# Kernel tuning notes

Measured on AMD Instinct MI355X. Metric: run time of the kernel, lower is better.

Reference implementation:

```python
import jax, jax.numpy as jnp
import numpy as np

NQ = 7
DIM = 2 ** NQ  # 128
N_LAYERS = 3

# Pauli-Z sign tables over the 128 basis states (wire 0 = most significant bit)
_bits = ((np.arange(DIM)[None, :] >> (NQ - 1 - np.arange(NQ)[:, None])) & 1)
_SZ = (1.0 - 2.0 * _bits).astype(np.float32)            # [7, 128]
_SZZ = (_SZ * np.roll(_SZ, -1, axis=0)).astype(np.float32)  # [7, 128], Z_i Z_{(i+1)%7}


def _cnot_perm(c, t):
    # CNOT is a basis-state permutation: flip target bit where control bit = 1
    k = np.arange(DIM)
    return k ^ (((k >> (NQ - 1 - c)) & 1) << (NQ - 1 - t))


def _apply_ry(state, theta, q):
    # state: [B, 128] complex64; theta: [B] or scalar (real)
    B = state.shape[0]
    s = state.reshape(B, 2 ** q, 2, 2 ** (NQ - 1 - q))
    c = jnp.reshape(jnp.cos(0.5 * theta), (-1, 1, 1))
    sn = jnp.reshape(jnp.sin(0.5 * theta), (-1, 1, 1))
    a0, a1 = s[:, :, 0, :], s[:, :, 1, :]
    return jnp.stack([c * a0 - sn * a1, sn * a0 + c * a1], axis=2).reshape(B, DIM)


def _apply_rz(state, theta, q):
    B = state.shape[0]
    s = state.reshape(B, 2 ** q, 2, 2 ** (NQ - 1 - q))
    p = jnp.reshape(jnp.exp(-0.5j * theta), (-1, 1, 1))  # diag(e^{-i t/2}, e^{+i t/2})
    return jnp.stack([p * s[:, :, 0, :], jnp.conj(p) * s[:, :, 1, :]], axis=2).reshape(B, DIM)


def _circuit(x_q, scales, biases, wry, wrz):
    # Batched 7-qubit state-vector simulation of quantum_circuit_v3
    B = x_q.shape[0]
    state = jnp.zeros((B, DIM), jnp.complex64).at[:, 0].set(1.0)
    ang = scales[None, :] * x_q + biases[None, :]  # [B, 7] encoding angles (same every layer)
    for layer in range(N_LAYERS):
        for i in range(NQ):
            state = _apply_ry(state, ang[:, i], i)
        for i in range(NQ):
            state = _apply_ry(state, wry[layer, i], i)
            state = _apply_rz(state, wrz[layer, i], i)
        shift = layer + 1
        for i in range(NQ):
            state = state[:, _cnot_perm(i, (i + shift) % NQ)]
    probs = state.real ** 2 + state.imag ** 2  # [B, 128]
    return jnp.concatenate([probs @ _SZ.T, probs @ _SZZ.T], axis=1)  # [B, 14]


def setup_inputs() -> dict:
    key = jax.random.key(0)
    ks = jax.random.split(key, 16)
    B, F = 32768, 64
    fus_in = 14 + 32 + F  # 110
    lin = lambda k, fi, fo: (0.05 * jax.random.normal(k, (fi, fo), jnp.float32))
    d = {
        "x_q": jax.random.uniform(ks[0], (B, NQ), jnp.float32),
        "x_c": jax.random.normal(ks[1], (B, F), jnp.float32),
        "input_scales": jnp.full((NQ,), np.pi, jnp.float32),
        "input_biases": jnp.zeros((NQ,), jnp.float32),
        "q_params_ry": 0.1 * jax.random.normal(ks[2], (N_LAYERS, NQ), jnp.float32),
        "q_params_rz": 0.1 * jax.random.normal(ks[3], (N_LAYERS, NQ), jnp.float32),
        "enc_w1": lin(ks[4], F, 64), "enc_b1": jnp.zeros((64,), jnp.float32),
        "enc_w2": lin(ks[5], 64, 32), "enc_b2": jnp.zeros((32,), jnp.float32),
        "fus_w1": lin(ks[6], fus_in, 128), "fus_b1": jnp.zeros((128,), jnp.float32),
        "fus_w2": lin(ks[7], 128, 64), "fus_b2": jnp.zeros((64,), jnp.float32),
        "fus_w3": lin(ks[8], 64, 32), "fus_b3": jnp.zeros((32,), jnp.float32),
        "fus_w4": lin(ks[9], 32, 1), "fus_b4": jnp.zeros((1,), jnp.float32),
    }
    return d


def reference(x_q, x_c, input_scales, input_biases, q_params_ry, q_params_rz,
              enc_w1, enc_b1, enc_w2, enc_b2,
              fus_w1, fus_b1, fus_w2, fus_b2, fus_w3, fus_b3, fus_w4, fus_b4):
    q_out = _circuit(x_q, input_scales, input_biases, q_params_ry, q_params_rz)  # [B, 14]
    h = jax.nn.relu(x_c @ enc_w1 + enc_b1)
    c_enc = jax.nn.relu(h @ enc_w2 + enc_b2)  # [B, 32]
    comb = jnp.concatenate([q_out, c_enc, x_c], axis=1)  # [B, 110]
    h = jax.nn.relu(comb @ fus_w1 + fus_b1)
    h = jax.nn.relu(h @ fus_w2 + fus_b2)
    h = jax.nn.relu(h @ fus_w3 + fus_b3)
    return (h @ fus_w4 + fus_b4)[:, 0]  # [B], dropout is identity at inference
```

## Files before the change

### kernel.cpp

```cpp
#include <hip/hip_runtime.h>
#include <math.h>

#define NQ 7
#define DIM 128
#define NLAYERS 3
#define ROWS 64
#define LDS_S 136

typedef __attribute__((ext_vector_type(8))) short bf16x8;
typedef __attribute__((ext_vector_type(4))) float f32x4;
typedef __attribute__((ext_vector_type(2))) float f32x2;
typedef __attribute__((ext_vector_type(4))) unsigned short us4;

__device__ __forceinline__ unsigned short f2bf(float x) {
    union { float f; unsigned int u; } v; v.f = x;
    unsigned int r = v.u + 0x7fff + ((v.u >> 16) & 1);
    return (unsigned short)(r >> 16);
}
__device__ __forceinline__ f32x2 sp(float x) { return (f32x2){x, x}; }
__device__ __forceinline__ f32x2 sel2(int c, f32x2 a, f32x2 b) {
    f32x2 r; r.x = c ? a.x : b.x; r.y = c ? a.y : b.y; return r;
}

constexpr int cperm(int k, int c, int t) {
    return k ^ (((k >> (6 - c)) & 1) << (6 - t));
}
constexpr int lgather(int k, int s) {
    int r = k;
    for (int i = 6; i >= 0; --i) r = cperm(r, i, (i + s) % 7);
    return r;
}

struct Mat { int c[7]; };

constexpr Mat ID{{1, 2, 4, 8, 16, 32, 64}};

constexpr int parity7(int x) { x ^= x >> 4; x ^= x >> 2; x ^= x >> 1; return x & 1; }

constexpr int mapv(const Mat& A, int v) {
    int r = 0;
    for (int j = 0; j < 7; ++j) if ((v >> j) & 1) r ^= A.c[j];
    return r;
}
constexpr Mat matmul(const Mat& A, const Mat& B) {
    Mat m{};
    for (int j = 0; j < 7; ++j) m.c[j] = mapv(A, B.c[j]);
    return m;
}
constexpr Mat matG(int L) {
    Mat m{};
    for (int j = 0; j < 7; ++j) m.c[j] = lgather(1 << j, L + 1);
    return m;
}
constexpr Mat matinv(const Mat& A) {
    int M[7] = {};
    for (int r = 0; r < 7; ++r) {
        int row = 0;
        for (int j = 0; j < 7; ++j) row |= ((A.c[j] >> r) & 1) << j;
        M[r] = row | (1 << (7 + r));
    }
    for (int col = 0; col < 7; ++col) {
        int piv = col;
        while (!((M[piv] >> col) & 1)) ++piv;
        int t = M[col]; M[col] = M[piv]; M[piv] = t;
        for (int r = 0; r < 7; ++r)
            if (r != col && ((M[r] >> col) & 1)) M[r] ^= M[col];
    }
    Mat inv{};
    for (int j = 0; j < 7; ++j) {
        int c = 0;
        for (int r = 0; r < 7; ++r) c |= ((M[r] >> (7 + j)) & 1) << r;
        inv.c[j] = c;
    }
    return inv;
}
constexpr bool isident(const Mat& A) {
    for (int j = 0; j < 7; ++j) if (A.c[j] != (1 << j)) return false;
    return true;
}

constexpr Mat LAM1  = matinv(matG(0));
constexpr Mat LAM2  = matmul(matinv(matG(1)), LAM1);
constexpr Mat LAM3  = matmul(matinv(matG(2)), LAM2);
constexpr Mat LAM1I = matG(0);
constexpr Mat LAM2I = matinv(LAM2);
static_assert(isident(matmul(LAM1, LAM1I)), "lam1 inv");
static_assert(isident(matmul(LAM2, LAM2I)), "lam2 inv");
static_assert(isident(matmul(matG(2), matmul(LAM3, matinv(LAM2)))), "lam3 chain");

constexpr int rowmask(const Mat& A, int b) {
    int r = 0;
    for (int j = 0; j < 7; ++j) r |= ((A.c[j] >> b) & 1) << j;
    return r;
}
constexpr int featM(const Mat& A, int m) {
    int M = 0;
    for (int j = 0; j < 7; ++j) M |= parity7(A.c[j] & m) << j;
    return M;
}
constexpr int szzmask(int i) { return (1 << (6 - i)) | (1 << (6 - ((i + 1) % 7))); }
constexpr int kmask(int k) { return (k < 7) ? (64 >> k) : szzmask(k - 7); }
constexpr unsigned pack_feat(int base) {
    unsigned r = 0;
    for (int j = 0; j < 4; ++j) {
        int k = base + j;
        unsigned e = (k < 14) ? (unsigned)featM(LAM3, kmask(k)) : 0u;
        r |= e << (8 * j);
    }
    return r;
}

template<int M>
__device__ __forceinline__ float xsh(float v) {
    if constexpr (M == 1 || M == 2 || M == 3) {
        constexpr int ctrl = (0 ^ M) | ((1 ^ M) << 2) | ((2 ^ M) << 4) | ((3 ^ M) << 6);
        return __int_as_float(__builtin_amdgcn_update_dpp(
            __float_as_int(v), __float_as_int(v), ctrl, 0xF, 0xF, true));
    } else if constexpr (M == 7) {
        return __int_as_float(__builtin_amdgcn_update_dpp(
            __float_as_int(v), __float_as_int(v), 0x141, 0xF, 0xF, true));
    } else if constexpr (M == 8) {
        return __int_as_float(__builtin_amdgcn_update_dpp(
            __float_as_int(v), __float_as_int(v), 0x128, 0xF, 0xF, true));
    } else if constexpr (M == 15) {
        return __int_as_float(__builtin_amdgcn_update_dpp(
            __float_as_int(v), __float_as_int(v), 0x140, 0xF, 0xF, true));
    } else if constexpr (M < 32) {
        return __int_as_float(__builtin_amdgcn_ds_swizzle(
            __float_as_int(v), (M << 10) | 0x1F));
    } else {
        return __shfl_xor(v, M, 64);
    }
}
template<int M>
__device__ __forceinline__ f32x2 xsh2(f32x2 v) {
    f32x2 r; r.x = xsh<M>(v.x); r.y = xsh<M>(v.y); return r;
}

__device__ __forceinline__ float bpermf(int addr, float v) {
    return __int_as_float(__builtin_amdgcn_ds_bpermute(addr, __float_as_int(v)));
}

template<int D, int R>
__device__ __forceinline__ void ryg(f32x2 c, f32x2 s, int lane,
                                    f32x2& x0r, f32x2& x0i, f32x2& x1r, f32x2& x1i)
{
    constexpr int  DL = D & 63;
    constexpr int  RL = R & 63;
    constexpr bool D6 = (D >> 6) & 1;
    constexpr bool R6 = (R >> 6) & 1;
    int par = __popc(lane & RL) & 1;
    f32x2 ns  = -s;
    f32x2 sg0 = sel2(par, s, ns);
    f32x2 sg1 = R6 ? sel2(par, ns, s) : sg0;
    f32x2 p0r, p0i, p1r, p1i;
    if constexpr (D6) {
        if constexpr (DL == 0) { p0r = x1r; p0i = x1i; p1r = x0r; p1i = x0i; }
        else {
            p0r = xsh2<DL>(x1r); p0i = xsh2<DL>(x1i);
            p1r = xsh2<DL>(x0r); p1i = xsh2<DL>(x0i);
        }
    } else {
        p0r = xsh2<DL>(x0r); p0i = xsh2<DL>(x0i);
        p1r = xsh2<DL>(x1r); p1i = xsh2<DL>(x1i);
    }
    x0r = c * x0r + sg0 * p0r;  x0i = c * x0i + sg0 * p0i;
    x1r = c * x1r + sg1 * p1r;  x1i = c * x1i + sg1 * p1i;
}

template<int LYR, int I>
__device__ __forceinline__ void rygates(
    const float* trig, const f32x2 (&dc)[NQ], const f32x2 (&dsn)[NQ], int lane,
    f32x2& A0r, f32x2& A0i, f32x2& A1r, f32x2& A1i)
{
    if constexpr (I < NQ) {
        constexpr Mat LM  = (LYR == 1) ? LAM1 : LAM2;
        constexpr Mat LMI = (LYR == 1) ? LAM1I : LAM2I;
        constexpr int b   = 6 - I;
        constexpr int D   = mapv(LMI, 1 << b);
        constexpr int R   = rowmask(LM, b);
        float cw = trig[(LYR * NQ + I) * 2 + 0];
        float sw = trig[(LYR * NQ + I) * 2 + 1];
        f32x2 c = dc[I] * sp(cw) - dsn[I] * sp(sw);
        f32x2 s = dsn[I] * sp(cw) + dc[I] * sp(sw);
        ryg<D, R>(c, s, lane, A0r, A0i, A1r, A1i);
        rygates<LYR, I + 1>(trig, dc, dsn, lane, A0r, A0i, A1r, A1i);
    }
}

template<int LYR, int Q>
__device__ __forceinline__ void rzrows(const float* __restrict__ wrz, int lane,
                                       float& Aacc, float& Bacc)
{
    if constexpr (Q < NQ) {
        constexpr Mat LM = (LYR == 0) ? ID : ((LYR == 1) ? LAM1 : LAM2);
        constexpr int R  = rowmask(LM, 6 - Q);
        float h = 0.5f * wrz[LYR * NQ + Q];
        float t = (__popc(lane & (R & 63)) & 1) ? -h : h;
        if constexpr ((R >> 6) & 1) Bacc += t; else Aacc += t;
        rzrows<LYR, Q + 1>(wrz, lane, Aacc, Bacc);
    }
}

template<int LYR>
__device__ __forceinline__ void rzlayer(const float* __restrict__ wrz, int lane,
    f32x2& A0r, f32x2& A0i, f32x2& A1r, f32x2& A1i)
{
    float Aacc = 0.0f, Bacc = 0.0f;
    rzrows<LYR, 0>(wrz, lane, Aacc, Bacc);
    float th0 = Aacc + Bacc, th1 = Aacc - Bacc;
    float c0 = __cosf(th0), s0 = __sinf(th0);
    float c1 = __cosf(th1), s1 = __sinf(th1);
    f32x2 r, im;
    r = A0r; im = A0i;
    A0r = sp(c0) * r  + sp(s0) * im;
    A0i = sp(c0) * im - sp(s0) * r;
    r = A1r; im = A1i;
    A1r = sp(c1) * r  + sp(s1) * im;
    A1i = sp(c1) * im - sp(s1) * r;
}

template<int M>
__device__ __forceinline__ void bfly2(int lane, f32x2& tp, f32x2& tm) {
    f32x2 pp = xsh2<M>(tp), pm = xsh2<M>(tm);
    int hi = lane & M;
    tp = sel2(hi, pp - tp, tp + pp);
    tm = sel2(hi, pm - tm, tm + pm);
}

__global__ __launch_bounds__(256) void circuit_kernel(
    const float* __restrict__ x_q, const float* __restrict__ scales,
    const float* __restrict__ biases,
    const float* __restrict__ wry, const float* __restrict__ wrz,
    const float* __restrict__ ew1, const float* __restrict__ ew2,
    const float* __restrict__ w1,  const float* __restrict__ w2,
    const float* __restrict__ w3,  const float* __restrict__ w4,
    float* __restrict__ q_out,
    unsigned short* __restrict__ ew1t, unsigned short* __restrict__ ew2t,
    unsigned short* __restrict__ w1t,  unsigned short* __restrict__ w2t,
    unsigned short* __restrict__ w3t,  unsigned short* __restrict__ w4t,
    int B)
{
    __shared__ float strig[NLAYERS * NQ * 2];
    const int tid  = threadIdx.x;
    const int lane = tid & 63;

    if (tid < NLAYERS * NQ) {
        float hy = 0.5f * wry[tid];
        strig[tid * 2 + 0] = __cosf(hy);
        strig[tid * 2 + 1] = __sinf(hy);
    }

    if (blockIdx.x < 64) {
        const int gbase  = blockIdx.x * 256 + tid;
        const int stride = 64 * 256;
        for (int i = gbase; i < 16384; i += stride) {
            int n = i >> 7, kp = i & 127;
            unsigned short v = 0;
            if (kp < 64)        v = f2bf(w1[(46 + kp) * 128 + n]);
            else if (kp < 78)   v = f2bf(w1[(kp - 64) * 128 + n]);
            else if (kp < 110)  v = f2bf(w1[(kp - 78 + 14) * 128 + n]);
            w1t[i] = v;
        }
        for (int i = gbase; i < 8192; i += stride) {
            int n = i >> 7, k = i & 127;
            w2t[i] = f2bf(w2[k * 64 + n]);
        }
        for (int i = gbase; i < 4096; i += stride) {
            int n = i >> 6, k = i & 63;
            ew1t[i] = f2bf(ew1[k * 64 + n]);
        }
        for (int i = gbase; i < 2048; i += stride) {
            int n = i >> 6, k = i & 63;
            ew2t[i] = f2bf(ew2[k * 32 + n]);
        }
        for (int i = gbase; i < 2048; i += stride) {
            int n = i >> 6, k = i & 63;
            w3t[i] = f2bf(w3[k * 32 + n]);
        }
        for (int i = gbase; i < 512; i += stride) {
            int n = i >> 5, k = i & 31;
            w4t[i] = (n == 0) ? f2bf(w4[k]) : (unsigned short)0;
        }
    }
    __syncthreads();

    int gtid = blockIdx.x * blockDim.x + tid;
    int wv   = gtid >> 6;
    int e0   = wv * 2;
    if (e0 >= B) return;

    f32x2 dc[NQ], dsn[NQ];
#pragma unroll
    for (int i = 0; i < NQ; ++i) {
        float h0 = 0.5f * fmaf(scales[i], x_q[(size_t)e0 * NQ + i], biases[i]);
        float h1 = 0.5f * fmaf(scales[i], x_q[(size_t)(e0 + 1) * NQ + i], biases[i]);
        dc[i]  = (f32x2){__cosf(h0), __cosf(h1)};
        dsn[i] = (f32x2){__sinf(h0), __sinf(h1)};
    }

    f32x2 A0r, A0i = sp(0.0f), A1r, A1i = sp(0.0f);
    {
        f32x2 cl[NQ], sl[NQ];
#pragma unroll
        for (int i = 0; i < NQ; ++i) {
            float cw = strig[i * 2 + 0], sw = strig[i * 2 + 1];
            cl[i] = dc[i] * sp(cw) - dsn[i] * sp(sw);
            sl[i] = dsn[i] * sp(cw) + dc[i] * sp(sw);
        }
        f32x2 f1 = sel2(lane & 32, sl[1], cl[1]);
        f32x2 f2 = sel2(lane & 16, sl[2], cl[2]);
        f32x2 f3 = sel2(lane &  8, sl[3], cl[3]);
        f32x2 f4 = sel2(lane &  4, sl[4], cl[4]);
        f32x2 f5 = sel2(lane &  2, sl[5], cl[5]);
        f32x2 f6 = sel2(lane &  1, sl[6], cl[6]);
        f32x2 pr = (f1 * f2) * (f3 * f4) * (f5 * f6);
        A0r = pr * cl[0];
        A1r = pr * sl[0];
    }

    rzlayer<0>(wrz, lane, A0r, A0i, A1r, A1i);
    rygates<1, 0>(strig, dc, dsn, lane, A0r, A0i, A1r, A1i);
    rzlayer<1>(wrz, lane, A0r, A0i, A1r, A1i);
    rygates<2, 0>(strig, dc, dsn, lane, A0r, A0i, A1r, A1i);
    rzlayer<2>(wrz, lane, A0r, A0i, A1r, A1i);

    f32x2 p0 = A0r * A0r + A0i * A0i;
    f32x2 p1 = A1r * A1r + A1i * A1i;
    f32x2 tp = p0 + p1;
    f32x2 tm = p0 - p1;

    bfly2<1>(lane, tp, tm);
    bfly2<2>(lane, tp, tm);
    bfly2<4>(lane, tp, tm);
    bfly2<8>(lane, tp, tm);
    bfly2<16>(lane, tp, tm);
    bfly2<32>(lane, tp, tm);

    {
        constexpr unsigned P0 = pack_feat(0),  P1 = pack_feat(4);
        constexpr unsigned P2 = pack_feat(8),  P3 = pack_feat(12);
        int k = lane & 15;
        unsigned wlo  = (k & 4) ? P1 : P0;
        unsigned whi  = (k & 4) ? P3 : P2;
        unsigned word = (k & 8) ? whi : wlo;
        unsigned entry = (word >> ((k & 3) * 8)) & 127u;
        int addr   = (int)(entry & 63u) << 2;
        int useTm  = (int)(entry & 64u);
        int e      = (lane >> 4) & 1;
        float vpx = bpermf(addr, tp.x), vpy = bpermf(addr, tp.y);
        float vmx = bpermf(addr, tm.x), vmy = bpermf(addr, tm.y);
        float vp = e ? vpy : vpx;
        float vm = e ? vmy : vmx;
        float val = useTm ? vm : vp;
        if (lane < 32) q_out[(size_t)e0 * 16 + lane] = val;
    }
}

template<int K, int NTILES, bool RELU>
__device__ __forceinline__ void layer_mfma(
    const unsigned short* src, unsigned short* dst,
    const unsigned short* __restrict__ wt, const float* __restrict__ bias,
    int dstcol, int lane, int wv)
{
    constexpr int KB   = K / 32;
    constexpr int NT_W = (NTILES > 4) ? NTILES / 4 : 1;
    constexpr int MT_W = NTILES / NT_W;
    const int ntile0 = (wv * NT_W) % NTILES;
    const int mtile0 = ((wv * NT_W) / NTILES) * MT_W;
    const int lcol = lane & 15;
    const int lrow = lane >> 4;

    bf16x8 bfrag[NT_W][KB];
    float  bb[NT_W];
#pragma unroll
    for (int n = 0; n < NT_W; ++n) {
#pragma unroll
        for (int kb = 0; kb < KB; ++kb)
            bfrag[n][kb] = *(const bf16x8*)&wt[((ntile0 + n) * 16 + lcol) * K + kb * 32 + lrow * 8];
        bb[n] = bias[(ntile0 + n) * 16 + lcol];
    }

#pragma unroll
    for (int m = 0; m < MT_W; ++m) {
        bf16x8 afrag[KB];
#pragma unroll
        for (int kb = 0; kb < KB; ++kb)
            afrag[kb] = *(const bf16x8*)&src[((mtile0 + m) * 16 + lcol) * LDS_S + kb * 32 + lrow * 8];

        f32x4 acc[NT_W];
#pragma unroll
        for (int n = 0; n < NT_W; ++n) acc[n] = (f32x4){bb[n], bb[n], bb[n], bb[n]};
#pragma unroll
        for (int kb = 0; kb < KB; ++kb)
#pragma unroll
            for (int n = 0; n < NT_W; ++n)
                acc[n] = __builtin_amdgcn_mfma_f32_16x16x32_bf16(afrag[kb], bfrag[n][kb], acc[n], 0, 0, 0);

#pragma unroll
        for (int n = 0; n < NT_W; ++n)
#pragma unroll
            for (int r = 0; r < 4; ++r) {
                float v = acc[n][r];
                if (RELU) v = fmaxf(v, 0.0f);
                dst[((mtile0 + m) * 16 + lrow * 4 + r) * LDS_S + dstcol + (ntile0 + n) * 16 + lcol] = f2bf(v);
            }
    }
}

__global__ __launch_bounds__(256, 4) void mlp_kernel(
    const float* __restrict__ q_out, const float* __restrict__ x_c,
    const unsigned short* __restrict__ ew1t, const float* __restrict__ eb1,
    const unsigned short* __restrict__ ew2t, const float* __restrict__ eb2,
    const unsigned short* __restrict__ w1t,  const float* __restrict__ b1,
    const unsigned short* __restrict__ w2t,  const float* __restrict__ b2,
    const unsigned short* __restrict__ w3t,  const float* __restrict__ b3,
    const unsigned short* __restrict__ w4t,  const float* __restrict__ b4,
    float* __restrict__ out, int B)
{
    __shared__ unsigned short BufA[ROWS * LDS_S];
    __shared__ unsigned short BufB[ROWS * LDS_S];

    const int tid  = threadIdx.x;
    const int lane = tid & 63;
    const int wv   = __builtin_amdgcn_readfirstlane(tid >> 6);
    const int base = blockIdx.x * ROWS;

    {
        const float4* xr = (const float4*)(x_c + (size_t)base * 64);
        for (int i = tid; i < 1024; i += 256) {
            int row = i >> 4, fc = i & 15;
            float4 v = xr[i];
            us4 b;
            b.x = f2bf(v.x); b.y = f2bf(v.y); b.z = f2bf(v.z); b.w = f2bf(v.w);
            *(us4*)&BufA[row * LDS_S + fc * 4] = b;
        }
    }
    for (int i = tid; i < 1024; i += 256) {
        int row = i >> 4, k = i & 15;
        BufA[row * LDS_S + 64 + k] = f2bf(q_out[(size_t)(base + row) * 16 + k]);
    }
    for (int i = tid; i < 64 * 18; i += 256) {
        int row = i / 18, k = i - row * 18;
        BufA[row * LDS_S + 110 + k] = 0;
    }
    __syncthreads();

    layer_mfma<64, 4, true>(BufA, BufB, ew1t, eb1, 0, lane, wv);
    __syncthreads();
    layer_mfma<64, 2, true>(BufB, BufA, ew2t, eb2, 78, lane, wv);
    __syncthreads();
    layer_mfma<128, 8, true>(BufA, BufB, w1t, b1, 0, lane, wv);
    __syncthreads();
    layer_mfma<128, 4, true>(BufB, BufA, w2t, b2, 0, lane, wv);
    __syncthreads();
    layer_mfma<64, 2, true>(BufA, BufB, w3t, b3, 0, lane, wv);
    __syncthreads();

    {
        const int lcol = lane & 15;
        const int lrow = lane >> 4;
        bf16x8 a = *(const bf16x8*)&BufB[(wv * 16 + lcol) * LDS_S + lrow * 8];
        bf16x8 b = *(const bf16x8*)&w4t[lcol * 32 + lrow * 8];
        float bv = b4[0];
        f32x4 acc = (f32x4){bv, bv, bv, bv};
        acc = __builtin_amdgcn_mfma_f32_16x16x32_bf16(a, b, acc, 0, 0, 0);
        if (lcol == 0) {
            float4 o; o.x = acc[0]; o.y = acc[1]; o.z = acc[2]; o.w = acc[3];
            *(float4*)(out + base + wv * 16 + lrow * 4) = o;
        }
    }
}

extern "C" void kernel_launch(void* const* d_in, const int* in_sizes, int n_in,
                              void* d_out, int out_size, void* d_ws, size_t ws_size,
                              hipStream_t stream)
{
    const float* x_q     = (const float*)d_in[0];
    const float* x_c     = (const float*)d_in[1];
    const float* scales  = (const float*)d_in[2];
    const float* biases  = (const float*)d_in[3];
    const float* wry     = (const float*)d_in[4];
    const float* wrz     = (const float*)d_in[5];
    const float* enc_w1  = (const float*)d_in[6];
    const float* enc_b1  = (const float*)d_in[7];
    const float* enc_w2  = (const float*)d_in[8];
    const float* enc_b2  = (const float*)d_in[9];
    const float* fus_w1  = (const float*)d_in[10];
    const float* fus_b1  = (const float*)d_in[11];
    const float* fus_w2  = (const float*)d_in[12];
    const float* fus_b2  = (const float*)d_in[13];
    const float* fus_w3  = (const float*)d_in[14];
    const float* fus_b3  = (const float*)d_in[15];
    const float* fus_w4  = (const float*)d_in[16];
    const float* fus_b4  = (const float*)d_in[17];
    float* out = (float*)d_out;

    int B = in_sizes[0] / NQ;

    float* ws    = (float*)d_ws;
    float* q_out = ws;
    unsigned short* wsh = (unsigned short*)(q_out + (size_t)B * 16);
    unsigned short* w1t  = wsh;
    unsigned short* w2t  = w1t + 16384;
    unsigned short* ew1t = w2t + 8192;
    unsigned short* ew2t = ew1t + 4096;
    unsigned short* w3t  = ew2t + 2048;
    unsigned short* w4t  = w3t + 2048;

    int circ_blocks = ((B / 2) * 64 + 255) / 256;
    circuit_kernel<<<circ_blocks, 256, 0, stream>>>(
        x_q, scales, biases, wry, wrz,
        enc_w1, enc_w2, fus_w1, fus_w2, fus_w3, fus_w4,
        q_out, ew1t, ew2t, w1t, w2t, w3t, w4t, B);

    int row_blocks = B / ROWS;
    mlp_kernel<<<row_blocks, 256, 0, stream>>>(q_out, x_c,
                                               ew1t, enc_b1, ew2t, enc_b2,
                                               w1t, fus_b1, w2t, fus_b2,
                                               w3t, fus_b3, w4t, fus_b4,
                                               out, B);
}
```

Baseline: 34.91 us.

## Precompute RZ phase tables in LDS and spread weight transpose across blocks

Each block now builds a per-layer table of cos/sin RZ phases for all 128 basis states in shared memory, so each thread reads four values from LDS instead of summing seven signed angles and calling four transcendentals per layer. The bf16 weight-transpose work, previously done by the first 64 blocks in strided loops, is now spread so that nine threads in every block each handle one element, loaded early and stored at the end of the kernel. This removes the load imbalance on the first blocks and the per-thread trig work, at the cost of every block computing the 384-entry table redundantly.

Measured after the change: 34.88 us. Within noise of the previous version (-0.1%).

```diff
diff --git a/kernel.cpp b/kernel.cpp
--- a/kernel.cpp
+++ b/kernel.cpp
@@ -188,29 +188,28 @@
     }
 }
 
-template<int LYR, int Q>
-__device__ __forceinline__ void rzrows(const float* __restrict__ wrz, int lane,
-                                       float& Aacc, float& Bacc)
+template<int L, int Q>
+__device__ __forceinline__ float rzph(const float* __restrict__ wrz, int p, float th)
 {
     if constexpr (Q < NQ) {
-        constexpr Mat LM = (LYR == 0) ? ID : ((LYR == 1) ? LAM1 : LAM2);
+        constexpr Mat LM = (L == 0) ? ID : ((L == 1) ? LAM1 : LAM2);
         constexpr int R  = rowmask(LM, 6 - Q);
-        float h = 0.5f * wrz[LYR * NQ + Q];
-        float t = (__popc(lane & (R & 63)) & 1) ? -h : h;
-        if constexpr ((R >> 6) & 1) Bacc += t; else Aacc += t;
-        rzrows<LYR, Q + 1>(wrz, lane, Aacc, Bacc);
+        float h = 0.5f * wrz[L * NQ + Q];
+        th += (__popc(R & p) & 1) ? -h : h;
+        return rzph<L, Q + 1>(wrz, p, th);
+    } else {
+        return th;
     }
 }
 
 template<int LYR>
-__device__ __forceinline__ void rzlayer(const float* __restrict__ wrz, int lane,
+__device__ __forceinline__ void rztab(const float* sphz, int lane,
     f32x2& A0r, f32x2& A0i, f32x2& A1r, f32x2& A1i)
 {
-    float Aacc = 0.0f, Bacc = 0.0f;
-    rzrows<LYR, 0>(wrz, lane, Aacc, Bacc);
-    float th0 = Aacc + Bacc, th1 = Aacc - Bacc;
-    float c0 = __cosf(th0), s0 = __sinf(th0);
-    float c1 = __cosf(th1), s1 = __sinf(th1);
+    float c0 = sphz[(LYR * 128 + lane) * 2 + 0];
+    float s0 = sphz[(LYR * 128 + lane) * 2 + 1];
+    float c1 = sphz[(LYR * 128 + 64 + lane) * 2 + 0];
+    float s1 = sphz[(LYR * 128 + 64 + lane) * 2 + 1];
     f32x2 r, im;
     r = A0r; im = A0i;
     A0r = sp(c0) * r  + sp(s0) * im;
@@ -242,53 +241,64 @@
     int B)
 {
     __shared__ float strig[NLAYERS * NQ * 2];
+    __shared__ float sphz[NLAYERS * 128 * 2];
     const int tid  = threadIdx.x;
     const int lane = tid & 63;
+
+    float trv = 0.0f;
+    unsigned short* trdst = nullptr;
+    {
+        int e = blockIdx.x * 9 + tid;
+        if (tid < 9 && e < 33280) {
+            const float* srcp = nullptr;
+            if (e < 16384) {
+                int n = e >> 7, kp = e & 127;
+                trdst = &w1t[e];
+                if (kp < 64)       srcp = &w1[(46 + kp) * 128 + n];
+                else if (kp < 78)  srcp = &w1[(kp - 64) * 128 + n];
+                else if (kp < 110) srcp = &w1[(kp - 78 + 14) * 128 + n];
+            } else if (e < 24576) {
+                int r = e - 16384, n = r >> 7, k = r & 127;
+                trdst = &w2t[r]; srcp = &w2[k * 64 + n];
+            } else if (e < 28672) {
+                int r = e - 24576, n = r >> 6, k = r & 63;
+                trdst = &ew1t[r]; srcp = &ew1[k * 64 + n];
+            } else if (e < 30720) {
+                int r = e - 28672, n = r >> 6, k = r & 63;
+                trdst = &ew2t[r]; srcp = &ew2[k * 32 + n];
+            } else if (e < 32768) {
+                int r = e - 30720, n = r >> 6, k = r & 63;
+                trdst = &w3t[r]; srcp = &w3[k * 32 + n];
+            } else {
+                int r = e - 32768, n = r >> 5, k = r & 31;
+                trdst = &w4t[r]; srcp = (n == 0) ? &w4[k] : nullptr;
+            }
+            if (srcp) trv = *srcp;
+        }
+    }
 
     if (tid < NLAYERS * NQ) {
         float hy = 0.5f * wry[tid];
         strig[tid * 2 + 0] = __cosf(hy);
         strig[tid * 2 + 1] = __sinf(hy);
     }
-
-    if (blockIdx.x < 64) {
-        const int gbase  = blockIdx.x * 256 + tid;
-        const int stride = 64 * 256;
-        for (int i = gbase; i < 16384; i += stride) {
-            int n = i >> 7, kp = i & 127;
-            unsigned short v = 0;
-            if (kp < 64)        v = f2bf(w1[(46 + kp) * 128 + n]);
-            else if (kp < 78)   v = f2bf(w1[(kp - 64) * 128 + n]);
-            else if (kp < 110)  v = f2bf(w1[(kp - 78 + 14) * 128 + n]);
-            w1t[i] = v;
-        }
-        for (int i = gbase; i < 8192; i += stride) {
-            int n = i >> 7, k = i & 127;
-            w2t[i] = f2bf(w2[k * 64 + n]);
-        }
-        for (int i = gbase; i < 4096; i += stride) {
-            int n = i >> 6, k = i & 63;
-            ew1t[i] = f2bf(ew1[k * 64 + n]);
-        }
-        for (int i = gbase; i < 2048; i += stride) {
-            int n = i >> 6, k = i & 63;
-            ew2t[i] = f2bf(ew2[k * 32 + n]);
-        }
-        for (int i = gbase; i < 2048; i += stride) {
-            int n = i >> 6, k = i & 63;
-            w3t[i] = f2bf(w3[k * 32 + n]);
-        }
-        for (int i = gbase; i < 512; i += stride) {
-            int n = i >> 5, k = i & 31;
-            w4t[i] = (n == 0) ? f2bf(w4[k]) : (unsigned short)0;
-        }
+    for (int e2 = tid; e2 < NLAYERS * 128; e2 += 256) {
+        int l = e2 >> 7, p = e2 & 127;
+        float th = (l == 0) ? rzph<0, 0>(wrz, p, 0.0f)
+                 : (l == 1) ? rzph<1, 0>(wrz, p, 0.0f)
+                            : rzph<2, 0>(wrz, p, 0.0f);
+        sphz[e2 * 2 + 0] = __cosf(th);
+        sphz[e2 * 2 + 1] = __sinf(th);
     }
     __syncthreads();
 
     int gtid = blockIdx.x * blockDim.x + tid;
     int wv   = gtid >> 6;
     int e0   = wv * 2;
-    if (e0 >= B) return;
+    if (e0 >= B) {
+        if (trdst) *trdst = f2bf(trv);
+        return;
+    }
 
     f32x2 dc[NQ], dsn[NQ];
 #pragma unroll
@@ -319,11 +329,11 @@
         A1r = pr * sl[0];
     }
 
-    rzlayer<0>(wrz, lane, A0r, A0i, A1r, A1i);
+    rztab<0>(sphz, lane, A0r, A0i, A1r, A1i);
     rygates<1, 0>(strig, dc, dsn, lane, A0r, A0i, A1r, A1i);
-    rzlayer<1>(wrz, lane, A0r, A0i, A1r, A1i);
+    rztab<1>(sphz, lane, A0r, A0i, A1r, A1i);
     rygates<2, 0>(strig, dc, dsn, lane, A0r, A0i, A1r, A1i);
-    rzlayer<2>(wrz, lane, A0r, A0i, A1r, A1i);
+    rztab<2>(sphz, lane, A0r, A0i, A1r, A1i);
 
     f32x2 p0 = A0r * A0r + A0i * A0i;
     f32x2 p1 = A1r * A1r + A1i * A1i;
@@ -355,6 +365,8 @@
         float val = useTm ? vm : vp;
         if (lane < 32) q_out[(size_t)e0 * 16 + lane] = val;
     }
+
+    if (trdst) *trdst = f2bf(trv);
 }
 
 template<int K, int NTILES, bool RELU>
```
